# Kernel tuning notes

Hardware: AMD Instinct MI355X
Metric: run time of the kernel (lower is better)

Reference implementation:

```python
import jax, jax.numpy as jnp
import numpy as np
import math

HEAD_DIM = 64

def setup_inputs() -> dict:
    key = jax.random.key(0)
    kq, kk, kv = jax.random.split(key, 3)
    B, H, S, D = 2, 16, 2048, HEAD_DIM
    Q = jax.random.normal(kq, (B, H, S, D), dtype=jnp.float32)
    K = jax.random.normal(kk, (B, H, S, D), dtype=jnp.float32)
    V = jax.random.normal(kv, (B, H, S, D), dtype=jnp.float32)
    mask = jnp.ones((B, S), dtype=jnp.float32)
    return {"Q": Q, "K": K, "V": V, "mask": mask}

def reference(Q, K, V, mask):
    # dot: [B, H, S, S]
    dot = jnp.einsum('bhqd,bhkd->bhqk', Q, K) / math.sqrt(HEAD_DIM)
    # additive mask: -1e6 where mask == 0 (mask broadcast over heads and query dim)
    dot = dot - 1000000.0 * (1.0 - mask[:, None, None, :])
    attn = jax.nn.softmax(dot, axis=-1)
    # dropout_prob = 0 -> identity
    X = jnp.einsum('bhqk,bhkd->bhqd', attn, V)
    return X
```

## Files before the change

### kernel.cpp

```cpp
#include <hip/hip_runtime.h>
#include <hip/hip_fp16.h>
#include <stdint.h>


#define S_LEN   2048
#define DHEAD   64
#define NPER    16
#define CEXP    9.0f
#define SCL2E   0.18033688011112042f
#define L2E     1.4426950408889634f

typedef __attribute__((ext_vector_type(4))) float    f32x4;
typedef __attribute__((ext_vector_type(2))) _Float16 f16x2;
typedef __attribute__((ext_vector_type(4))) _Float16 f16x4;
typedef __attribute__((ext_vector_type(8))) _Float16 f16x8;
typedef __attribute__((ext_vector_type(2))) __fp16   hf16x2;

static __device__ __forceinline__ float exp2_fast(float x) {
#if __has_builtin(__builtin_amdgcn_exp2f)
  return __builtin_amdgcn_exp2f(x);
#else
  float r;
  asm("v_exp_f32 %0, %1" : "=v"(r) : "v"(x));
  return r;
#endif
}

static __device__ __forceinline__ hf16x2 pkh(float a, float b) {
  return __builtin_amdgcn_cvt_pkrtz(a, b);
}
static __device__ __forceinline__ f16x2 h2f(hf16x2 h) {
  union { hf16x2 i; f16x2 o; } u; u.i = h; return u.o;
}

#define GLDS16(g, l)                                                  \
  __builtin_amdgcn_global_load_lds(                                   \
      (const __attribute__((address_space(1))) void*)(g),             \
      (__attribute__((address_space(3))) void*)(l), 16, 0, 0)

__global__ __launch_bounds__(256) void prep(
    const float* __restrict__ K, const float* __restrict__ V,
    const float* __restrict__ Mk, _Float16* __restrict__ Kswz,
    _Float16* __restrict__ Vg, float* __restrict__ madd_g) {
  const int gb = blockIdx.x;
  if (gb < 2048) {
    const int idx = gb * 256 + threadIdx.x;
    const int c  = idx & 7;
    const int kv = (idx >> 3) & 2047;
    const int bh = idx >> 14;
    const float* src = K + ((size_t)bh * S_LEN + kv) * DHEAD + c * 8;
    float4 a = *(const float4*)(src);
    float4 d = *(const float4*)(src + 4);
    union { f16x2 h[4]; f16x8 v; } r;
    r.h[0] = h2f(pkh(a.x, a.y)); r.h[1] = h2f(pkh(a.z, a.w));
    r.h[2] = h2f(pkh(d.x, d.y)); r.h[3] = h2f(pkh(d.z, d.w));
    *(f16x8*)(Kswz + ((size_t)bh * S_LEN + kv) * DHEAD + ((c + kv) & 7) * 8) = r.v;
    if (idx < 2 * S_LEN)
      madd_g[idx] = -CEXP - (1.0e6f * L2E) * (1.0f - Mk[idx]);
  } else {
    const int idx = (gb - 2048) * 256 + threadIdx.x;
    const int d  = idx & 63;
    const int g  = (idx >> 6) & 15;
    const int j  = (idx >> 10) & 31;
    const int bh = idx >> 15;
    const float* src = V + ((size_t)bh * S_LEN + j * 64 + g * 4) * DHEAD + d;
    float v0 = src[0], v1 = src[64], v2 = src[128], v3 = src[192];
    union { f16x2 h[2]; f16x4 v; } r;
    r.h[0] = h2f(pkh(v0, v1)); r.h[1] = h2f(pkh(v2, v3));
    *(f16x4*)(Vg + (size_t)idx * 4) = r.v;
  }
}

__global__ __launch_bounds__(256, 2) void attn_ws(
    const float* __restrict__ Q, const _Float16* __restrict__ Kswz,
    const _Float16* __restrict__ Vg, const float* __restrict__ madd_g,
    float* __restrict__ O) {
  __shared__ __align__(16) _Float16 kls[2][2][4096];
  __shared__ __align__(16) _Float16 vls[2][2][4096];
  __shared__ __align__(16) float    mls[2][2][64];

  const int tid  = threadIdx.x;
  const int lane = tid & 63;
  const int wave = tid >> 6;
  const int quad = lane >> 4;
  const int x    = lane & 15;

  const int blk  = blockIdx.x;
  const int bh   = (blk & 7) | (((blk >> 3) & 3) << 3);
  const int qblk = blk >> 5;
  const int b    = bh >> 4;

  const size_t base = (size_t)bh * S_LEN * DHEAD;
  const float*    Qb = Q + base;
  const _Float16* Kb = Kswz + base;
  const _Float16* Vb = Vg + base;
  const float*    Mb = madd_g + b * S_LEN;
  float* Ob = O + base;

  const int q0 = qblk * 128 + wave * 16 + x;
  f16x8 qf[2][2];
#pragma unroll
  for (int u = 0; u < 2; ++u) {
    const float* qp = Qb + (size_t)(q0 + u * 64) * DHEAD + quad * 8;
#pragma unroll
    for (int kb = 0; kb < 2; ++kb) {
      float4 a = *(const float4*)(qp + kb * 32);
      float4 c = *(const float4*)(qp + kb * 32 + 4);
      union { f16x2 h[4]; f16x8 v; } r;
      r.h[0] = h2f(pkh(a.x * SCL2E, a.y * SCL2E));
      r.h[1] = h2f(pkh(a.z * SCL2E, a.w * SCL2E));
      r.h[2] = h2f(pkh(c.x * SCL2E, c.y * SCL2E));
      r.h[3] = h2f(pkh(c.z * SCL2E, c.w * SCL2E));
      qf[u][kb] = r.v;
    }
  }

  auto prefetch = [&](int p, int bi) {
    const _Float16* ks = Kb + p * 8192 + tid * 8;
    const _Float16* vs = Vb + p * 8192 + tid * 8;
    _Float16* kd = &kls[bi][0][tid * 8];
    _Float16* vd = &vls[bi][0][tid * 8];
    GLDS16(ks,        kd);
    GLDS16(ks + 2048, kd + 2048);
    GLDS16(ks + 4096, kd + 4096);
    GLDS16(ks + 6144, kd + 6144);
    GLDS16(vs,        vd);
    GLDS16(vs + 2048, vd + 2048);
    GLDS16(vs + 4096, vd + 4096);
    GLDS16(vs + 6144, vd + 6144);
    if (tid < 32)
      GLDS16(Mb + p * 128 + tid * 4, &mls[bi][0][tid * 4]);
  };

  f32x4 xacc[2][4];
#pragma unroll
  for (int u = 0; u < 2; ++u)
#pragma unroll
    for (int m = 0; m < 4; ++m) xacc[u][m] = (f32x4){0.f, 0.f, 0.f, 0.f};
  float lsum[2] = {0.0f, 0.0f};
  const hf16x2 one2 = {(__fp16)1.0f, (__fp16)1.0f};

  prefetch(0, 0);
  __syncthreads();

  for (int p = 0; p < NPER; ++p) {
    const int cur = p & 1;
    if (p + 1 < NPER) prefetch(p + 1, cur ^ 1);

#pragma unroll
    for (int sub = 0; sub < 2; ++sub) {
      const _Float16* k0 = &kls[cur][sub][x * 64 + ((quad + x) & 7) * 8];
      const _Float16* k1 = &kls[cur][sub][x * 64 + ((quad + 4 + x) & 7) * 8];
      const float*    mp = &mls[cur][sub][quad * 4];
      f16x4 pf[2][4];
#pragma unroll
      for (int t = 0; t < 4; ++t) {
        f16x8 ka0 = *(const f16x8*)(k0 + t * 1024);
        f16x8 ka1 = *(const f16x8*)(k1 + t * 1024);
        f32x4 mi = *(const f32x4*)(mp + t * 16);
#pragma unroll
        for (int u = 0; u < 2; ++u) {
          f32x4 st = __builtin_amdgcn_mfma_f32_16x16x32_f16(ka0, qf[u][0], mi, 0, 0, 0);
          st = __builtin_amdgcn_mfma_f32_16x16x32_f16(ka1, qf[u][1], st, 0, 0, 0);
          hf16x2 h0 = pkh(exp2_fast(st.x), exp2_fast(st.y));
          hf16x2 h1 = pkh(exp2_fast(st.z), exp2_fast(st.w));
#if __has_builtin(__builtin_amdgcn_fdot2)
          lsum[u] = __builtin_amdgcn_fdot2(h0, one2, lsum[u], false);
          lsum[u] = __builtin_amdgcn_fdot2(h1, one2, lsum[u], false);
#else
          f16x2 a0 = h2f(h0), a1 = h2f(h1);
          lsum[u] += (float)a0.x + (float)a0.y + (float)a1.x + (float)a1.y;
#endif
          union { f16x2 h[2]; f16x4 v; } r;
          r.h[0] = h2f(h0);
          r.h[1] = h2f(h1);
          pf[u][t] = r.v;
        }
      }
      const _Float16* vbase = &vls[cur][sub][256 * quad + 4 * x];
#pragma unroll
      for (int m = 0; m < 4; ++m) {
        f32x4 x0 = xacc[0][m];
        f32x4 x1 = xacc[1][m];
#pragma unroll
        for (int t = 0; t < 4; ++t) {
          f16x4 vf = *(const f16x4*)(vbase + 1024 * t + 64 * m);
          x0 = __builtin_amdgcn_mfma_f32_16x16x16f16(vf, pf[0][t], x0, 0, 0, 0);
          x1 = __builtin_amdgcn_mfma_f32_16x16x16f16(vf, pf[1][t], x1, 0, 0, 0);
        }
        xacc[0][m] = x0;
        xacc[1][m] = x1;
      }
    }
    __syncthreads();
  }

#pragma unroll
  for (int u = 0; u < 2; ++u) {
    float l = lsum[u];
    l += __shfl_xor(l, 16, 64);
    l += __shfl_xor(l, 32, 64);
    const float rl = 1.0f / l;
    float* op = Ob + (size_t)(q0 + u * 64) * DHEAD;
#pragma unroll
    for (int m = 0; m < 4; ++m) {
      float4 o;
      o.x = xacc[u][m].x * rl; o.y = xacc[u][m].y * rl;
      o.z = xacc[u][m].z * rl; o.w = xacc[u][m].w * rl;
      *(float4*)(op + m * 16 + quad * 4) = o;
    }
  }
}

extern "C" void kernel_launch(void* const* d_in, const int* in_sizes, int n_in,
                              void* d_out, int out_size, void* d_ws, size_t ws_size,
                              hipStream_t stream) {
  const float* Q = (const float*)d_in[0];
  const float* K = (const float*)d_in[1];
  const float* V = (const float*)d_in[2];
  const float* M = (const float*)d_in[3];
  float* O = (float*)d_out;

  _Float16* Kswz = (_Float16*)d_ws;
  _Float16* Vg   = Kswz + 4194304;
  float*    madd = (float*)((char*)d_ws + 16777216);
  hipLaunchKernelGGL(prep, dim3(6144), dim3(256), 0, stream, K, V, M, Kswz, Vg, madd);
  hipLaunchKernelGGL(attn_ws, dim3(512), dim3(256), 0, stream, Q, Kswz, Vg, madd, O);
}
```

Measured before the change: 137.8 us.

## Split KV sequence across two wave teams per block and merge partials

Doubles the block to 512 threads with two teams of four waves. Each team handles half the key/value sequence, 1024 keys, in 64-key chunks, so each wave does half the serial KV loop. At the end, team 1 writes its partial accumulators and row sums to shared memory and team 0 combines them and writes the output. This raises per-CU wave parallelism and shortens the per-wave loop, at the cost of a final shared-memory reduction, an extra barrier, and smaller per-iteration loads with more barriers per unit of work.

```diff
diff --git a/kernel.cpp b/kernel.cpp
--- a/kernel.cpp
+++ b/kernel.cpp
@@ -71,7 +71,7 @@
   }
 }
 
-__global__ __launch_bounds__(256, 2) void attn_ws(
+__global__ __launch_bounds__(512, 4) void attn_ws(
     const float* __restrict__ Q, const _Float16* __restrict__ Kswz,
     const _Float16* __restrict__ Vg, const float* __restrict__ madd_g,
     float* __restrict__ O) {
@@ -82,6 +82,9 @@
   const int tid  = threadIdx.x;
   const int lane = tid & 63;
   const int wave = tid >> 6;
+  const int team = wave >> 2;
+  const int twav = wave & 3;
+  const int ttid = tid & 255;
   const int quad = lane >> 4;
   const int x    = lane & 15;
 
@@ -97,7 +100,7 @@
   const float*    Mb = madd_g + b * S_LEN;
   float* Ob = O + base;
 
-  const int q0 = qblk * 128 + wave * 16 + x;
+  const int q0 = qblk * 128 + twav * 16 + x;
   f16x8 qf[2][2];
 #pragma unroll
   for (int u = 0; u < 2; ++u) {
@@ -116,20 +119,17 @@
   }
 
   auto prefetch = [&](int p, int bi) {
-    const _Float16* ks = Kb + p * 8192 + tid * 8;
-    const _Float16* vs = Vb + p * 8192 + tid * 8;
-    _Float16* kd = &kls[bi][0][tid * 8];
-    _Float16* vd = &vls[bi][0][tid * 8];
+    const int j = team * NPER + p;
+    const _Float16* ks = Kb + j * 4096 + ttid * 8;
+    const _Float16* vs = Vb + j * 4096 + ttid * 8;
+    _Float16* kd = &kls[team][bi][ttid * 8];
+    _Float16* vd = &vls[team][bi][ttid * 8];
     GLDS16(ks,        kd);
     GLDS16(ks + 2048, kd + 2048);
-    GLDS16(ks + 4096, kd + 4096);
-    GLDS16(ks + 6144, kd + 6144);
     GLDS16(vs,        vd);
     GLDS16(vs + 2048, vd + 2048);
-    GLDS16(vs + 4096, vd + 4096);
-    GLDS16(vs + 6144, vd + 6144);
-    if (tid < 32)
-      GLDS16(Mb + p * 128 + tid * 4, &mls[bi][0][tid * 4]);
+    if (ttid < 16)
+      GLDS16(Mb + team * 1024 + p * 64 + ttid * 4, &mls[team][bi][ttid * 4]);
   };
 
   f32x4 xacc[2][4];
@@ -147,67 +147,86 @@
     const int cur = p & 1;
     if (p + 1 < NPER) prefetch(p + 1, cur ^ 1);
 
-#pragma unroll
-    for (int sub = 0; sub < 2; ++sub) {
-      const _Float16* k0 = &kls[cur][sub][x * 64 + ((quad + x) & 7) * 8];
-      const _Float16* k1 = &kls[cur][sub][x * 64 + ((quad + 4 + x) & 7) * 8];
-      const float*    mp = &mls[cur][sub][quad * 4];
-      f16x4 pf[2][4];
+    const _Float16* k0 = &kls[team][cur][x * 64 + ((quad + x) & 7) * 8];
+    const _Float16* k1 = &kls[team][cur][x * 64 + ((quad + 4 + x) & 7) * 8];
+    const float*    mp = &mls[team][cur][quad * 4];
+    f16x4 pf[2][4];
+#pragma unroll
+    for (int t = 0; t < 4; ++t) {
+      f16x8 ka0 = *(const f16x8*)(k0 + t * 1024);
+      f16x8 ka1 = *(const f16x8*)(k1 + t * 1024);
+      f32x4 mi = *(const f32x4*)(mp + t * 16);
+#pragma unroll
+      for (int u = 0; u < 2; ++u) {
+        f32x4 st = __builtin_amdgcn_mfma_f32_16x16x32_f16(ka0, qf[u][0], mi, 0, 0, 0);
+        st = __builtin_amdgcn_mfma_f32_16x16x32_f16(ka1, qf[u][1], st, 0, 0, 0);
+        hf16x2 h0 = pkh(exp2_fast(st.x), exp2_fast(st.y));
+        hf16x2 h1 = pkh(exp2_fast(st.z), exp2_fast(st.w));
+#if __has_builtin(__builtin_amdgcn_fdot2)
+        lsum[u] = __builtin_amdgcn_fdot2(h0, one2, lsum[u], false);
+        lsum[u] = __builtin_amdgcn_fdot2(h1, one2, lsum[u], false);
+#else
+        f16x2 a0 = h2f(h0), a1 = h2f(h1);
+        lsum[u] += (float)a0.x + (float)a0.y + (float)a1.x + (float)a1.y;
+#endif
+        union { f16x2 h[2]; f16x4 v; } r;
+        r.h[0] = h2f(h0);
+        r.h[1] = h2f(h1);
+        pf[u][t] = r.v;
+      }
+    }
+    const _Float16* vbase = &vls[team][cur][256 * quad + 4 * x];
+#pragma unroll
+    for (int m = 0; m < 4; ++m) {
+      f32x4 x0 = xacc[0][m];
+      f32x4 x1 = xacc[1][m];
 #pragma unroll
       for (int t = 0; t < 4; ++t) {
-        f16x8 ka0 = *(const f16x8*)(k0 + t * 1024);
-        f16x8 ka1 = *(const f16x8*)(k1 + t * 1024);
-        f32x4 mi = *(const f32x4*)(mp + t * 16);
-#pragma unroll
-        for (int u = 0; u < 2; ++u) {
-          f32x4 st = __builtin_amdgcn_mfma_f32_16x16x32_f16(ka0, qf[u][0], mi, 0, 0, 0);
-          st = __builtin_amdgcn_mfma_f32_16x16x32_f16(ka1, qf[u][1], st, 0, 0, 0);
-          hf16x2 h0 = pkh(exp2_fast(st.x), exp2_fast(st.y));
-          hf16x2 h1 = pkh(exp2_fast(st.z), exp2_fast(st.w));
-#if __has_builtin(__builtin_amdgcn_fdot2)
-          lsum[u] = __builtin_amdgcn_fdot2(h0, one2, lsum[u], false);
-          lsum[u] = __builtin_amdgcn_fdot2(h1, one2, lsum[u], false);
-#else
-          f16x2 a0 = h2f(h0), a1 = h2f(h1);
-          lsum[u] += (float)a0.x + (float)a0.y + (float)a1.x + (float)a1.y;
-#endif
-          union { f16x2 h[2]; f16x4 v; } r;
-          r.h[0] = h2f(h0);
-          r.h[1] = h2f(h1);
-          pf[u][t] = r.v;
-        }
+        f16x4 vf = *(const f16x4*)(vbase + 1024 * t + 64 * m);
+        x0 = __builtin_amdgcn_mfma_f32_16x16x16f16(vf, pf[0][t], x0, 0, 0, 0);
+        x1 = __builtin_amdgcn_mfma_f32_16x16x16f16(vf, pf[1][t], x1, 0, 0, 0);
       }
-      const _Float16* vbase = &vls[cur][sub][256 * quad + 4 * x];
+      xacc[0][m] = x0;
+      xacc[1][m] = x1;
+    }
+    __syncthreads();
+  }
+
+#pragma unroll
+  for (int u = 0; u < 2; ++u) {
+    lsum[u] += __shfl_xor(lsum[u], 16, 64);
+    lsum[u] += __shfl_xor(lsum[u], 32, 64);
+  }
+
+  float* sx = (float*)&kls[0][0][0];
+  float* sl = (float*)&vls[0][0][0];
+  if (team == 1) {
+#pragma unroll
+    for (int u = 0; u < 2; ++u) {
+#pragma unroll
+      for (int m = 0; m < 4; ++m)
+        *(f32x4*)&sx[(u * 4 + m) * 1024 + ttid * 4] = xacc[u][m];
+      sl[ttid * 2 + u] = lsum[u];
+    }
+  }
+  __syncthreads();
+  if (team == 0) {
+#pragma unroll
+    for (int u = 0; u < 2; ++u) {
+      const float l = lsum[u] + sl[ttid * 2 + u];
+      const float rl = 1.0f / l;
+      float* op = Ob + (size_t)(q0 + u * 64) * DHEAD;
 #pragma unroll
       for (int m = 0; m < 4; ++m) {
-        f32x4 x0 = xacc[0][m];
-        f32x4 x1 = xacc[1][m];
-#pragma unroll
-        for (int t = 0; t < 4; ++t) {
-          f16x4 vf = *(const f16x4*)(vbase + 1024 * t + 64 * m);
-          x0 = __builtin_amdgcn_mfma_f32_16x16x16f16(vf, pf[0][t], x0, 0, 0, 0);
-          x1 = __builtin_amdgcn_mfma_f32_16x16x16f16(vf, pf[1][t], x1, 0, 0, 0);
-        }
-        xacc[0][m] = x0;
-        xacc[1][m] = x1;
+        f32x4 xo = xacc[u][m];
+        f32x4 xr = *(const f32x4*)&sx[(u * 4 + m) * 1024 + ttid * 4];
+        float4 o;
+        o.x = (xo.x + xr.x) * rl;
+        o.y = (xo.y + xr.y) * rl;
+        o.z = (xo.z + xr.z) * rl;
+        o.w = (xo.w + xr.w) * rl;
+        *(float4*)(op + m * 16 + quad * 4) = o;
       }
-    }
-    __syncthreads();
-  }
-
-#pragma unroll
-  for (int u = 0; u < 2; ++u) {
-    float l = lsum[u];
-    l += __shfl_xor(l, 16, 64);
-    l += __shfl_xor(l, 32, 64);
-    const float rl = 1.0f / l;
-    float* op = Ob + (size_t)(q0 + u * 64) * DHEAD;
-#pragma unroll
-    for (int m = 0; m < 4; ++m) {
-      float4 o;
-      o.x = xacc[u][m].x * rl; o.y = xacc[u][m].y * rl;
-      o.z = xacc[u][m].z * rl; o.w = xacc[u][m].w * rl;
-      *(float4*)(op + m * 16 + quad * 4) = o;
     }
   }
 }
@@ -225,5 +244,5 @@
   _Float16* Vg   = Kswz + 4194304;
   float*    madd = (float*)((char*)d_ws + 16777216);
   hipLaunchKernelGGL(prep, dim3(6144), dim3(256), 0, stream, K, V, M, Kswz, Vg, madd);
-  hipLaunchKernelGGL(attn_ws, dim3(512), dim3(256), 0, stream, Q, Kswz, Vg, madd, O);
-}
+  hipLaunchKernelGGL(attn_ws, dim3(512), dim3(512), 0, stream, Q, Kswz, Vg, madd, O);
+}
```

Measured after the change: 138.6 us. About the same (+0.6%).
